# Optimization experiments

Measured on AMD Instinct MI355X. Metric: run time of the kernel, lower is better.

## Reference

```python
import jax, jax.numpy as jnp
import numpy as np
import math

B, H, S, D = 4, 16, 2048, 128

def setup_inputs() -> dict:
    key = jax.random.key(0)
    kq, kk, kv = jax.random.split(key, 3)
    query = jax.random.normal(kq, (B, H, S, D), dtype=jnp.float32)
    k = jax.random.normal(kk, (B, H, S, D), dtype=jnp.float32)
    value = jax.random.normal(kv, (B, H, S, D), dtype=jnp.float32)
    attn_mask = jnp.tril(jnp.ones((S, S), dtype=bool))  # causal
    key_padding_mask = jnp.ones((B, S), dtype=bool)      # all keys valid
    return {"query": query, "key": k, "value": value,
            "attn_mask": attn_mask, "key_padding_mask": key_padding_mask}

def reference(query, key, value, attn_mask, key_padding_mask):
    dk = query.shape[-1]
    # [B,H,Sq,Sk]
    scores = jnp.einsum('bhqd,bhkd->bhqk', query, key) / math.sqrt(dk)
    fill = jnp.finfo(scores.dtype).min
    # attn_mask [Sq,Sk] -> [1,1,Sq,Sk]; True = keep
    scores = jnp.where(attn_mask[None, None, :, :], scores, fill)
    # key_padding_mask [B,Sk] -> [B,1,1,Sk]; True = keep
    scores = jnp.where(key_padding_mask[:, None, None, :], scores, fill)
    attn = jax.nn.softmax(scores, axis=-1)
    # dropout p=0.0 / eval mode -> identity
    return jnp.einsum('bhqk,bhkd->bhqd', attn, value)
```

## Files before the change

kernel.cpp:

```cpp
#include <hip/hip_runtime.h>
#include <hip/hip_bf16.h>
#include <math.h>

#define S_LEN 2048
#define D_DIM 128
#define NHEADS 64

typedef unsigned short u16;
typedef __attribute__((ext_vector_type(8))) short bf16x8;
typedef __attribute__((ext_vector_type(4))) float f32x4;
typedef __attribute__((ext_vector_type(16))) float f32x16;

__device__ __forceinline__ u16 f2b(float f) {
  union { float f; unsigned u; } v; v.f = f;
  return (u16)((v.u + 0x7fffu + ((v.u >> 16) & 1u)) >> 16);
}
__device__ __forceinline__ unsigned pkbf(float a, float b) {
  unsigned au = __float_as_uint(a) + 0x8000u;
  unsigned bu = __float_as_uint(b) + 0x8000u;
  return (au >> 16) | (bu & 0xffff0000u);
}
__device__ __forceinline__ void pl32swap(unsigned &a, unsigned &b) {
  asm("v_permlane32_swap_b32 %0, %1" : "+v"(a), "+v"(b));
}
__device__ __forceinline__ f32x16 z16() {
  f32x16 v;
  #pragma unroll
  for (int i = 0; i < 16; ++i) v[i] = 0.f;
  return v;
}

#define GLL16(g, l) __builtin_amdgcn_global_load_lds(                       \
    (const __attribute__((address_space(1))) unsigned*)(g),                 \
    (__attribute__((address_space(3))) unsigned*)(l), 16, 0, 0)

__global__ __launch_bounds__(256, 2)
void conv_kernel(const float* __restrict__ K, const float* __restrict__ V,
                 u16* __restrict__ Kws, u16* __restrict__ Vws) {
  __shared__ __align__(16) u16 VL[128 * 72];
  const int h = blockIdx.x >> 3;
  const int s = blockIdx.x & 7;
  const int tid = threadIdx.x;
  const size_t hb = (size_t)h * S_LEN * D_DIM;
  const float* Kb = K + hb;
  const float* Vb = V + hb;
  u16* Ko = Kws + hb;
  u16* Vo = Vws + hb;

  #pragma unroll 2
  for (int it = 0; it < 16; ++it) {
    int idx = it * 256 + tid;
    int k = 256 * s + (idx >> 4), g = idx & 15;
    const float* src = Kb + (size_t)k * D_DIM + 8 * g;
    float4 a = *(const float4*)src;
    float4 b = *(const float4*)(src + 4);
    bf16x8 f;
    f[0]=f2b(a.x); f[1]=f2b(a.y); f[2]=f2b(a.z); f[3]=f2b(a.w);
    f[4]=f2b(b.x); f[5]=f2b(b.y); f[6]=f2b(b.z); f[7]=f2b(b.w);
    *(bf16x8*)&Ko[(size_t)k * D_DIM + 8 * g] = f;
  }
  for (int tt = 0; tt < 4; ++tt) {
    const int k0t = 256 * s + 64 * tt;
    __syncthreads();
    #pragma unroll 2
    for (int it = 0; it < 8; ++it) {
      int idx = it * 256 + tid;
      int row = idx >> 5, c4 = idx & 31;
      float4 v = *(const float4*)(Vb + (size_t)(k0t + row) * D_DIM + 4 * c4);
      VL[(4*c4 + 0) * 72 + row] = f2b(v.x);
      VL[(4*c4 + 1) * 72 + row] = f2b(v.y);
      VL[(4*c4 + 2) * 72 + row] = f2b(v.z);
      VL[(4*c4 + 3) * 72 + row] = f2b(v.w);
    }
    __syncthreads();
    #pragma unroll
    for (int it = 0; it < 4; ++it) {
      int idx = it * 256 + tid;
      int d = idx >> 3, kc = idx & 7;
      bf16x8 f = *(const bf16x8*)&VL[d * 72 + 8 * kc];
      *(bf16x8*)&Vo[(size_t)d * S_LEN + k0t + 8 * kc] = f;
    }
  }
}

__global__ __launch_bounds__(256, 2)
void fattn32(const float* __restrict__ Qg, const u16* __restrict__ Kws,
             const u16* __restrict__ Vws, float* __restrict__ Og) {
  __shared__ __align__(16) u16 Kl[2][8192];
  __shared__ __align__(16) u16 Vl[2][8192];

  const int tid = threadIdx.x, lane = tid & 63, w = tid >> 6;
  const int l31 = lane & 31, hi = lane >> 5;
  const int kx = l31 & 7;

  const int L = blockIdx.x;
  const int xcd = L & 7, slot = L >> 3;
  const int head = xcd * 8 + (slot >> 3);
  const int pr = slot & 7;

  const size_t hb = (size_t)head * S_LEN * D_DIM;
  const float* Qb = Qg + hb;
  float*       Ob = Og + hb;
  const u16*   Kh = Kws + hb;
  const u16*   Vh = Vws + hb;

  int cur = 0;

  auto stage = [&](int buf, int t) {
    const int k0 = t * 64;
    #pragma unroll
    for (int j = 0; j < 4; ++j) {
      const int sb = (j * 4 + w) * 64;
      {
        int sk = sb + lane;
        int k = sk >> 4, gs = sk & 15, g = gs ^ (k & 7);
        GLL16(Kh + (size_t)(k0 + k) * D_DIM + 8 * g, &Kl[buf][sb * 8]);
      }
      {
        int sv = sb + lane;
        int d = sv >> 3, gks = sv & 7, gk = gks ^ (d & 7);
        GLL16(Vh + (size_t)d * S_LEN + k0 + 8 * gk, &Vl[buf][sb * 8]);
      }
    }
  };

  #pragma unroll 1
  for (int qi = 0; qi < 2; ++qi) {
    const int qt  = qi ? pr : (15 - pr);
    const int q0w = qt * 128 + 32 * w;
    const int ntk = 2 * qt + 2;
    const int myq = q0w + l31;

    bf16x8 qf[8];
    {
      const float sc = 0.12753139f;
      const float* qp = Qb + (size_t)myq * D_DIM + 8 * hi;
      #pragma unroll
      for (int c = 0; c < 8; ++c) {
        float4 a = *(const float4*)(qp + 16 * c);
        float4 b = *(const float4*)(qp + 16 * c + 4);
        bf16x8 f;
        f[0]=f2b(a.x*sc); f[1]=f2b(a.y*sc); f[2]=f2b(a.z*sc); f[3]=f2b(a.w*sc);
        f[4]=f2b(b.x*sc); f[5]=f2b(b.y*sc); f[6]=f2b(b.z*sc); f[7]=f2b(b.w*sc);
        qf[c] = f;
      }
    }

    f32x16 oa0 = z16(), oa1 = z16(), oa2 = z16(), oa3 = z16();
    float m_run = 0.f, l_run = 0.f;

    stage(cur, 0);
    __syncthreads();

    #pragma unroll 1
    for (int t = 0; t < ntk; ++t) {
      if (t + 1 < ntk) stage(cur ^ 1, t + 1);

      if (64 * t <= q0w + 31) {
        const u16* K8 = &Kl[cur][0];
        const u16* V8 = &Vl[cur][0];

        f32x16 s0 = z16(), s1 = z16();
        __builtin_amdgcn_s_setprio(1);
        #pragma unroll
        for (int c = 0; c < 8; ++c) {
          const int gs = (c * 2 + hi) ^ kx;
          bf16x8 ka = *(const bf16x8*)&K8[ l31       * 128 + gs * 8];
          bf16x8 kb = *(const bf16x8*)&K8[(32 + l31) * 128 + gs * 8];
          s0 = __builtin_amdgcn_mfma_f32_32x32x16_bf16(ka, qf[c], s0, 0,0,0);
          s1 = __builtin_amdgcn_mfma_f32_32x32x16_bf16(kb, qf[c], s1, 0,0,0);
        }
        __builtin_amdgcn_s_setprio(0);

        if (64 * t + 63 > q0w) {
          const int qm = myq - 64 * t;
          #pragma unroll
          for (int i = 0; i < 16; ++i) {
            const int kr = (i & 3) + 8 * (i >> 2) + 4 * hi;
            if (kr > qm)      s0[i] = -1e30f;
            if (32 + kr > qm) s1[i] = -1e30f;
          }
        }

        float tm[16];
        #pragma unroll
        for (int i = 0; i < 16; ++i) tm[i] = fmaxf(s0[i], s1[i]);
        #pragma unroll
        for (int st = 8; st >= 1; st >>= 1)
          #pragma unroll
          for (int i = 0; i < 8; ++i) if (i < st) tm[i] = fmaxf(tm[i], tm[i+st]);
        float mx = fmaxf(tm[0], __shfl_xor(tm[0], 32));

        if (mx > m_run + 8.0f) {
          float corr = exp2f(m_run - mx);
          #pragma unroll
          for (int i = 0; i < 16; ++i) {
            oa0[i] *= corr; oa1[i] *= corr; oa2[i] *= corr; oa3[i] *= corr;
          }
          l_run *= corr; m_run = mx;
        }

        float ps0 = 0.f, ps1 = 0.f, ps2 = 0.f, ps3 = 0.f;
        #pragma unroll
        for (int i = 0; i < 16; ++i) {
          float p0 = exp2f(s0[i] - m_run);
          float p1 = exp2f(s1[i] - m_run);
          s0[i] = p0; s1[i] = p1;
          if ((i & 3) == 0) { ps0 += p0; ps1 += p1; }
          else if ((i & 3) == 1) { ps2 += p0; ps3 += p1; }
          else if ((i & 3) == 2) { ps0 += p0; ps1 += p1; }
          else { ps2 += p0; ps3 += p1; }
        }
        l_run += (ps0 + ps1) + (ps2 + ps3);

        unsigned w0[8], w1[8];
        #pragma unroll
        for (int j = 0; j < 8; ++j) {
          w0[j] = pkbf(s0[2*j], s0[2*j+1]);
          w1[j] = pkbf(s1[2*j], s1[2*j+1]);
        }
        pl32swap(w0[0], w0[2]); pl32swap(w0[1], w0[3]);
        pl32swap(w0[4], w0[6]); pl32swap(w0[5], w0[7]);
        pl32swap(w1[0], w1[2]); pl32swap(w1[1], w1[3]);
        pl32swap(w1[4], w1[6]); pl32swap(w1[5], w1[7]);
        union { unsigned u[4]; bf16x8 v; } pf[4];
        pf[0].u[0]=w0[0]; pf[0].u[1]=w0[1]; pf[0].u[2]=w0[2]; pf[0].u[3]=w0[3];
        pf[1].u[0]=w0[4]; pf[1].u[1]=w0[5]; pf[1].u[2]=w0[6]; pf[1].u[3]=w0[7];
        pf[2].u[0]=w1[0]; pf[2].u[1]=w1[1]; pf[2].u[2]=w1[2]; pf[2].u[3]=w1[3];
        pf[3].u[0]=w1[4]; pf[3].u[1]=w1[5]; pf[3].u[2]=w1[6]; pf[3].u[3]=w1[7];

        __builtin_amdgcn_s_setprio(1);
        #pragma unroll
        for (int c = 0; c < 4; ++c) {
          const int gv = (c * 2 + hi) ^ kx;
          bf16x8 v0 = *(const bf16x8*)&V8[( l31      ) * 64 + gv * 8];
          bf16x8 v1 = *(const bf16x8*)&V8[( 32 + l31 ) * 64 + gv * 8];
          bf16x8 v2 = *(const bf16x8*)&V8[( 64 + l31 ) * 64 + gv * 8];
          bf16x8 v3 = *(const bf16x8*)&V8[( 96 + l31 ) * 64 + gv * 8];
          oa0 = __builtin_amdgcn_mfma_f32_32x32x16_bf16(v0, pf[c].v, oa0, 0,0,0);
          oa1 = __builtin_amdgcn_mfma_f32_32x32x16_bf16(v1, pf[c].v, oa1, 0,0,0);
          oa2 = __builtin_amdgcn_mfma_f32_32x32x16_bf16(v2, pf[c].v, oa2, 0,0,0);
          oa3 = __builtin_amdgcn_mfma_f32_32x32x16_bf16(v3, pf[c].v, oa3, 0,0,0);
        }
        __builtin_amdgcn_s_setprio(0);
      }

      __syncthreads();
      cur ^= 1;
    }

    float l_tot = l_run + __shfl_xor(l_run, 32);
    float inv = 1.0f / l_tot;
    float* op = Ob + (size_t)myq * D_DIM;
    #pragma unroll
    for (int i = 0; i < 16; ++i) {
      const int d = (i & 3) + 8 * (i >> 2) + 4 * hi;
      op[d]      = oa0[i] * inv;
      op[32 + d] = oa1[i] * inv;
      op[64 + d] = oa2[i] * inv;
      op[96 + d] = oa3[i] * inv;
    }
  }
}

__global__ __launch_bounds__(256, 3)
void fattn_v2(const float* __restrict__ Qg, const float* __restrict__ Kg,
              const float* __restrict__ Vg, float* __restrict__ Og) {
  __shared__ __align__(16) u16 K8[16 * 64 * 8];
  __shared__ __align__(16) u16 V8[8 * 128 * 8];
  __shared__ __align__(16) u16 Plf[4 * 16 * 72];
  const int tid = threadIdx.x, lane = tid & 63, w = tid >> 6;
  const int lr = lane & 15, lg = lane >> 4;
  const int qtile = blockIdx.x % 32, bh = blockIdx.x / 32;
  const int q0 = qtile * 64;
  const size_t base = (size_t)bh * S_LEN * D_DIM;
  const float *Qb = Qg + base, *Kb = Kg + base, *Vb = Vg + base;
  float* Ob = Og + base;
  bf16x8 qf[4];
  {
    const float* qp = Qb + (size_t)(q0 + w * 16 + lr) * D_DIM + lg * 8;
    #pragma unroll
    for (int cc = 0; cc < 4; ++cc) {
      float4 a = *(const float4*)(qp + cc * 32);
      float4 b = *(const float4*)(qp + cc * 32 + 4);
      bf16x8 f;
      f[0]=f2b(a.x); f[1]=f2b(a.y); f[2]=f2b(a.z); f[3]=f2b(a.w);
      f[4]=f2b(b.x); f[5]=f2b(b.y); f[6]=f2b(b.z); f[7]=f2b(b.w);
      qf[cc] = f;
    }
  }
  f32x4 oacc[8];
  #pragma unroll
  for (int c = 0; c < 8; ++c) oacc[c] = (f32x4){0.f,0.f,0.f,0.f};
  float m_run[4] = {-INFINITY,-INFINITY,-INFINITY,-INFINITY};
  float l_run[4] = {0.f,0.f,0.f,0.f};
  const int sg_ = tid >> 5, dq_ = tid & 31;
  float4 kb[8], vb[8];
  auto prefetch = [&](int k0) {
    const float* kp = Kb + (size_t)(k0 + lane) * D_DIM;
    #pragma unroll
    for (int i = 0; i < 4; ++i) {
      int dg = w + 4 * i;
      kb[2*i]   = *(const float4*)(kp + dg * 8);
      kb[2*i+1] = *(const float4*)(kp + dg * 8 + 4);
    }
    #pragma unroll
    for (int jj = 0; jj < 8; ++jj) {
      int row = k0 + (jj & 3) * 16 + 2 * sg_ + (jj >> 2);
      vb[jj] = *(const float4*)(Vb + (size_t)row * D_DIM + dq_ * 4);
    }
  };
  const int ntiles = qtile + 1;
  const float scale = 0.08838834764831845f;
  prefetch(0);
  for (int t = 0; t < ntiles; ++t) {
    #pragma unroll
    for (int i = 0; i < 4; ++i) {
      int dg = w + 4 * i;
      float4 a = kb[2*i], b = kb[2*i+1];
      bf16x8 f;
      f[0]=f2b(a.x); f[1]=f2b(a.y); f[2]=f2b(a.z); f[3]=f2b(a.w);
      f[4]=f2b(b.x); f[5]=f2b(b.y); f[6]=f2b(b.z); f[7]=f2b(b.w);
      *(bf16x8*)&K8[(dg * 64 + lane) * 8] = f;
    }
    #pragma unroll
    for (int dd = 0; dd < 4; ++dd) {
      bf16x8 f;
      #pragma unroll
      for (int jj = 0; jj < 8; ++jj) {
        float c = (dd==0)?vb[jj].x:(dd==1)?vb[jj].y:(dd==2)?vb[jj].z:vb[jj].w;
        f[jj] = f2b(c);
      }
      *(bf16x8*)&V8[(sg_ * 128 + dq_ * 4 + dd) * 8] = f;
    }
    __syncthreads();
    if (t + 1 < ntiles) prefetch((t + 1) * 64);
    const bool diag = (t == qtile);
    f32x4 sa[4];
    #pragma unroll
    for (int c = 0; c < 4; ++c) sa[c] = (f32x4){0.f,0.f,0.f,0.f};
    #pragma unroll
    for (int cc = 0; cc < 4; ++cc) {
      #pragma unroll
      for (int c = 0; c < 4; ++c) {
        bf16x8 kf = *(const bf16x8*)&K8[((cc*4+lg)*64 + c*16 + lr)*8];
        sa[c] = __builtin_amdgcn_mfma_f32_16x16x32_bf16(qf[cc], kf, sa[c], 0,0,0);
      }
    }
    #pragma unroll
    for (int r = 0; r < 4; ++r) {
      float s0=sa[0][r]*scale, s1=sa[1][r]*scale, s2=sa[2][r]*scale, s3=sa[3][r]*scale;
      if (diag) {
        int lim = 16*w + lg*4 + r;
        if (     lr > lim) s0 = -INFINITY;
        if (16 + lr > lim) s1 = -INFINITY;
        if (32 + lr > lim) s2 = -INFINITY;
        if (48 + lr > lim) s3 = -INFINITY;
      }
      float mx = fmaxf(fmaxf(s0,s1), fmaxf(s2,s3));
      #pragma unroll
      for (int d = 1; d < 16; d <<= 1) mx = fmaxf(mx, __shfl_xor(mx, d));
      float mn = fmaxf(m_run[r], mx);
      float corr = __expf(m_run[r] - mn);
      float p0=__expf(s0-mn), p1=__expf(s1-mn), p2=__expf(s2-mn), p3=__expf(s3-mn);
      float ps = (p0+p1)+(p2+p3);
      #pragma unroll
      for (int d = 1; d < 16; d <<= 1) ps += __shfl_xor(ps, d);
      l_run[r] = l_run[r]*corr + ps;
      m_run[r] = mn;
      #pragma unroll
      for (int c = 0; c < 8; ++c) oacc[c][r] *= corr;
      ushort4 pw = make_ushort4(f2b(p0), f2b(p1), f2b(p2), f2b(p3));
      *(ushort4*)&Plf[((w*16 + lg*4 + r) * 72) + 4*lr] = pw;
    }
    #pragma unroll
    for (int pass = 0; pass < 2; ++pass) {
      bf16x8 pfv = *(const bf16x8*)&Plf[(w*16 + lr)*72 + pass*32 + lg*8];
      #pragma unroll
      for (int c = 0; c < 8; ++c) {
        bf16x8 vf = *(const bf16x8*)&V8[((pass*4 + lg)*128 + c*16 + lr)*8];
        oacc[c] = __builtin_amdgcn_mfma_f32_16x16x32_bf16(pfv, vf, oacc[c], 0,0,0);
      }
    }
    __syncthreads();
  }
  #pragma unroll
  for (int r = 0; r < 4; ++r) {
    const int mq = q0 + w*16 + lg*4 + r;
    const float inv = 1.0f / l_run[r];
    float* op = Ob + (size_t)mq * D_DIM + lr;
    #pragma unroll
    for (int c = 0; c < 8; ++c) op[c*16] = oacc[c][r] * inv;
  }
}

extern "C" void kernel_launch(void* const* d_in, const int* in_sizes, int n_in,
                              void* d_out, int out_size, void* d_ws, size_t ws_size,
                              hipStream_t stream) {
  const float* Q = (const float*)d_in[0];
  const float* K = (const float*)d_in[1];
  const float* V = (const float*)d_in[2];
  float* O = (float*)d_out;
  const size_t elems = (size_t)NHEADS * S_LEN * D_DIM;
  const size_t need = 2 * elems * sizeof(u16);
  if (ws_size >= need) {
    u16* Kws = (u16*)d_ws;
    u16* Vws = Kws + elems;
    conv_kernel<<<dim3(512), dim3(256), 0, stream>>>(K, V, Kws, Vws);
    fattn32<<<dim3(512), dim3(256), 0, stream>>>(Q, Kws, Vws, O);
  } else {
    fattn_v2<<<dim3(NHEADS * 32), dim3(256), 0, stream>>>(Q, K, V, O);
  }
}
```

Measured before the change: 163.9 us.

## Use 8-wave blocks with triple-buffered K/V staging and one barrier per tile

Workgroups grow from 4 to 8 waves, so each block covers a 256-row query tile and K/V tiles loaded into LDS serve twice as many queries. The double-buffered LDS ring becomes a triple buffer. Loads are issued two tiles ahead, and explicit vmcnt waits plus a single barrier per iteration replace the two __syncthreads. Together these aim to cut global/LDS traffic per query and hide load latency. The cost is 96KB of LDS per block, half as many blocks, and a coarser split of causal work across blocks.

```diff
diff --git a/kernel.cpp b/kernel.cpp
--- a/kernel.cpp
+++ b/kernel.cpp
@@ -83,11 +83,11 @@
   }
 }
 
-__global__ __launch_bounds__(256, 2)
-void fattn32(const float* __restrict__ Qg, const u16* __restrict__ Kws,
+__global__ __launch_bounds__(512, 2)
+void fattn8w(const float* __restrict__ Qg, const u16* __restrict__ Kws,
              const u16* __restrict__ Vws, float* __restrict__ Og) {
-  __shared__ __align__(16) u16 Kl[2][8192];
-  __shared__ __align__(16) u16 Vl[2][8192];
+  __shared__ __align__(16) u16 Kl[3][8192];
+  __shared__ __align__(16) u16 Vl[3][8192];
 
   const int tid = threadIdx.x, lane = tid & 63, w = tid >> 6;
   const int l31 = lane & 31, hi = lane >> 5;
@@ -95,8 +95,8 @@
 
   const int L = blockIdx.x;
   const int xcd = L & 7, slot = L >> 3;
-  const int head = xcd * 8 + (slot >> 3);
-  const int pr = slot & 7;
+  const int head = xcd * 8 + (slot >> 2);
+  const int pr = slot & 3;
 
   const size_t hb = (size_t)head * S_LEN * D_DIM;
   const float* Qb = Qg + hb;
@@ -104,13 +104,11 @@
   const u16*   Kh = Kws + hb;
   const u16*   Vh = Vws + hb;
 
-  int cur = 0;
-
   auto stage = [&](int buf, int t) {
     const int k0 = t * 64;
     #pragma unroll
-    for (int j = 0; j < 4; ++j) {
-      const int sb = (j * 4 + w) * 64;
+    for (int j = 0; j < 2; ++j) {
+      const int sb = (w * 2 + j) * 64;
       {
         int sk = sb + lane;
         int k = sk >> 4, gs = sk & 15, g = gs ^ (k & 7);
@@ -126,9 +124,9 @@
 
   #pragma unroll 1
   for (int qi = 0; qi < 2; ++qi) {
-    const int qt  = qi ? pr : (15 - pr);
-    const int q0w = qt * 128 + 32 * w;
-    const int ntk = 2 * qt + 2;
+    const int qt  = qi ? pr : (7 - pr);
+    const int q0w = qt * 256 + 32 * w;
+    const int ntk = 4 * qt + 4;
     const int myq = q0w + l31;
 
     bf16x8 qf[8];
@@ -149,16 +147,20 @@
     f32x16 oa0 = z16(), oa1 = z16(), oa2 = z16(), oa3 = z16();
     float m_run = 0.f, l_run = 0.f;
 
-    stage(cur, 0);
-    __syncthreads();
+    stage(0, 0);
+    stage(1, 1);
+    int rb = 0;
 
     #pragma unroll 1
     for (int t = 0; t < ntk; ++t) {
-      if (t + 1 < ntk) stage(cur ^ 1, t + 1);
+      if (t + 1 < ntk) asm volatile("s_waitcnt vmcnt(4)" ::: "memory");
+      else             asm volatile("s_waitcnt vmcnt(0)" ::: "memory");
+      __builtin_amdgcn_s_barrier();
+      asm volatile("" ::: "memory");
 
       if (64 * t <= q0w + 31) {
-        const u16* K8 = &Kl[cur][0];
-        const u16* V8 = &Vl[cur][0];
+        const u16* K8 = &Kl[rb][0];
+        const u16* V8 = &Vl[rb][0];
 
         f32x16 s0 = z16(), s1 = z16();
         __builtin_amdgcn_s_setprio(1);
@@ -245,8 +247,12 @@
         __builtin_amdgcn_s_setprio(0);
       }
 
-      __syncthreads();
-      cur ^= 1;
+      if (t + 2 < ntk) {
+        int nb = rb + 2; if (nb >= 3) nb -= 3;
+        stage(nb, t + 2);
+      }
+      asm volatile("" ::: "memory");
+      rb = (rb + 1 == 3) ? 0 : rb + 1;
     }
 
     float l_tot = l_run + __shfl_xor(l_run, 32);
@@ -260,6 +266,7 @@
       op[64 + d] = oa2[i] * inv;
       op[96 + d] = oa3[i] * inv;
     }
+    __builtin_amdgcn_s_barrier();
   }
 }
 
@@ -407,7 +414,7 @@
     u16* Kws = (u16*)d_ws;
     u16* Vws = Kws + elems;
     conv_kernel<<<dim3(512), dim3(256), 0, stream>>>(K, V, Kws, Vws);
-    fattn32<<<dim3(512), dim3(256), 0, stream>>>(Q, Kws, Vws, O);
+    fattn8w<<<dim3(256), dim3(512), 0, stream>>>(Q, Kws, Vws, O);
   } else {
     fattn_v2<<<dim3(NHEADS * 32), dim3(256), 0, stream>>>(Q, K, V, O);
   }
```

Measured after the change: 156.0 us. 4.8% less time.

## Split each key tile across two wave groups with LDS softmax merge

Applied to the files above, without the earlier changes.

Blocks grow from 256 to 512 threads. Each 32-row query strip is now handled by two waves that each process one 32-key half of every 64-key tile, and their partial output accumulators and running max/sum statistics are merged through LDS at the end. The bit-trick bf16 packing is replaced by the hardware v_cvt_pk_bf16_f32 instruction, and the per-tile sync becomes an explicit vmcnt wait plus barrier. The aim is more waves in flight per CU and shorter dependency chains per wave. The cost is extra LDS traffic and barriers for the final merge, plus higher register and occupancy pressure from the 512-thread launch bounds.

```diff
diff --git a/kernel.cpp b/kernel.cpp
--- a/kernel.cpp
+++ b/kernel.cpp
@@ -15,10 +15,10 @@
   union { float f; unsigned u; } v; v.f = f;
   return (u16)((v.u + 0x7fffu + ((v.u >> 16) & 1u)) >> 16);
 }
-__device__ __forceinline__ unsigned pkbf(float a, float b) {
-  unsigned au = __float_as_uint(a) + 0x8000u;
-  unsigned bu = __float_as_uint(b) + 0x8000u;
-  return (au >> 16) | (bu & 0xffff0000u);
+__device__ __forceinline__ unsigned cvtpk(float lo, float hi) {
+  unsigned r;
+  asm("v_cvt_pk_bf16_f32 %0, %1, %2" : "=v"(r) : "v"(lo), "v"(hi));
+  return r;
 }
 __device__ __forceinline__ void pl32swap(unsigned &a, unsigned &b) {
   asm("v_permlane32_swap_b32 %0, %1" : "+v"(a), "+v"(b));
@@ -83,15 +83,18 @@
   }
 }
 
-__global__ __launch_bounds__(256, 2)
-void fattn32(const float* __restrict__ Qg, const u16* __restrict__ Kws,
-             const u16* __restrict__ Vws, float* __restrict__ Og) {
-  __shared__ __align__(16) u16 Kl[2][8192];
-  __shared__ __align__(16) u16 Vl[2][8192];
+__global__ __launch_bounds__(512, 4)
+void fattn_ps(const float* __restrict__ Qg, const u16* __restrict__ Kws,
+              const u16* __restrict__ Vws, float* __restrict__ Og) {
+  __shared__ __align__(16) u16 Kl[2][2][4096];
+  __shared__ __align__(16) u16 Vl[2][2][4096];
+  __shared__ float ML[4][64];
 
   const int tid = threadIdx.x, lane = tid & 63, w = tid >> 6;
   const int l31 = lane & 31, hi = lane >> 5;
   const int kx = l31 & 7;
+  const int vx = (l31 >> 1) & 3;
+  const int strip = w & 3, par = w >> 2;
 
   const int L = blockIdx.x;
   const int xcd = L & 7, slot = L >> 3;
@@ -104,30 +107,21 @@
   const u16*   Kh = Kws + hb;
   const u16*   Vh = Vws + hb;
 
-  int cur = 0;
-
   auto stage = [&](int buf, int t) {
     const int k0 = t * 64;
     #pragma unroll
-    for (int j = 0; j < 4; ++j) {
-      const int sb = (j * 4 + w) * 64;
-      {
-        int sk = sb + lane;
-        int k = sk >> 4, gs = sk & 15, g = gs ^ (k & 7);
-        GLL16(Kh + (size_t)(k0 + k) * D_DIM + 8 * g, &Kl[buf][sb * 8]);
-      }
-      {
-        int sv = sb + lane;
-        int d = sv >> 3, gks = sv & 7, gk = gks ^ (d & 7);
-        GLL16(Vh + (size_t)d * S_LEN + k0 + 8 * gk, &Vl[buf][sb * 8]);
-      }
+    for (int j = 0; j < 2; ++j) {
+      { int k = tid >> 4, gs = tid & 15, g = gs ^ (k & 7);
+        GLL16(Kh + (size_t)(k0 + 32*j + k) * D_DIM + 8 * g, &Kl[buf][j][tid * 8]); }
+      { int d = tid >> 2, gks = tid & 3, gk = gks ^ ((d >> 1) & 3);
+        GLL16(Vh + (size_t)d * S_LEN + (k0 + 32*j) + 8 * gk, &Vl[buf][j][tid * 8]); }
     }
   };
 
   #pragma unroll 1
   for (int qi = 0; qi < 2; ++qi) {
     const int qt  = qi ? pr : (15 - pr);
-    const int q0w = qt * 128 + 32 * w;
+    const int q0w = qt * 128 + 32 * strip;
     const int ntk = 2 * qt + 2;
     const int myq = q0w + l31;
 
@@ -149,47 +143,47 @@
     f32x16 oa0 = z16(), oa1 = z16(), oa2 = z16(), oa3 = z16();
     float m_run = 0.f, l_run = 0.f;
 
-    stage(cur, 0);
-    __syncthreads();
+    stage(0, 0);
 
     #pragma unroll 1
     for (int t = 0; t < ntk; ++t) {
-      if (t + 1 < ntk) stage(cur ^ 1, t + 1);
-
-      if (64 * t <= q0w + 31) {
-        const u16* K8 = &Kl[cur][0];
-        const u16* V8 = &Vl[cur][0];
-
-        f32x16 s0 = z16(), s1 = z16();
+      asm volatile("s_waitcnt vmcnt(0)" ::: "memory");
+      __builtin_amdgcn_s_barrier();
+      asm volatile("" ::: "memory");
+      if (t + 1 < ntk) stage((t + 1) & 1, t + 1);
+
+      const int k0p = 64 * t + 32 * par;
+      if (k0p <= q0w + 31) {
+        const u16* K8 = &Kl[t & 1][par][0];
+        const u16* V8 = &Vl[t & 1][par][0];
+
+        f32x16 s = z16();
         __builtin_amdgcn_s_setprio(1);
         #pragma unroll
         for (int c = 0; c < 8; ++c) {
-          const int gs = (c * 2 + hi) ^ kx;
-          bf16x8 ka = *(const bf16x8*)&K8[ l31       * 128 + gs * 8];
-          bf16x8 kb = *(const bf16x8*)&K8[(32 + l31) * 128 + gs * 8];
-          s0 = __builtin_amdgcn_mfma_f32_32x32x16_bf16(ka, qf[c], s0, 0,0,0);
-          s1 = __builtin_amdgcn_mfma_f32_32x32x16_bf16(kb, qf[c], s1, 0,0,0);
+          const int gs = (2 * c + hi) ^ kx;
+          bf16x8 ka = *(const bf16x8*)&K8[(l31 * 16 + gs) * 8];
+          s = __builtin_amdgcn_mfma_f32_32x32x16_bf16(ka, qf[c], s, 0, 0, 0);
         }
         __builtin_amdgcn_s_setprio(0);
 
-        if (64 * t + 63 > q0w) {
-          const int qm = myq - 64 * t;
+        if (k0p + 31 > q0w) {
+          const int qm = myq - k0p;
           #pragma unroll
           for (int i = 0; i < 16; ++i) {
             const int kr = (i & 3) + 8 * (i >> 2) + 4 * hi;
-            if (kr > qm)      s0[i] = -1e30f;
-            if (32 + kr > qm) s1[i] = -1e30f;
+            if (kr > qm) s[i] = -1e30f;
           }
         }
 
-        float tm[16];
-        #pragma unroll
-        for (int i = 0; i < 16; ++i) tm[i] = fmaxf(s0[i], s1[i]);
-        #pragma unroll
-        for (int st = 8; st >= 1; st >>= 1)
-          #pragma unroll
-          for (int i = 0; i < 8; ++i) if (i < st) tm[i] = fmaxf(tm[i], tm[i+st]);
-        float mx = fmaxf(tm[0], __shfl_xor(tm[0], 32));
+        float t0 = fmaxf(s[0], s[1]),  t1 = fmaxf(s[2], s[3]);
+        float t2 = fmaxf(s[4], s[5]),  t3 = fmaxf(s[6], s[7]);
+        float t4 = fmaxf(s[8], s[9]),  t5 = fmaxf(s[10], s[11]);
+        float t6 = fmaxf(s[12], s[13]), t7 = fmaxf(s[14], s[15]);
+        t0 = fmaxf(fmaxf(t0, t1), fmaxf(t2, t3));
+        t4 = fmaxf(fmaxf(t4, t5), fmaxf(t6, t7));
+        float mx = fmaxf(t0, t4);
+        mx = fmaxf(mx, __shfl_xor(mx, 32));
 
         if (mx > m_run + 8.0f) {
           float corr = exp2f(m_run - mx);
@@ -200,66 +194,72 @@
           l_run *= corr; m_run = mx;
         }
 
-        float ps0 = 0.f, ps1 = 0.f, ps2 = 0.f, ps3 = 0.f;
-        #pragma unroll
-        for (int i = 0; i < 16; ++i) {
-          float p0 = exp2f(s0[i] - m_run);
-          float p1 = exp2f(s1[i] - m_run);
-          s0[i] = p0; s1[i] = p1;
-          if ((i & 3) == 0) { ps0 += p0; ps1 += p1; }
-          else if ((i & 3) == 1) { ps2 += p0; ps3 += p1; }
-          else if ((i & 3) == 2) { ps0 += p0; ps1 += p1; }
-          else { ps2 += p0; ps3 += p1; }
-        }
-        l_run += (ps0 + ps1) + (ps2 + ps3);
-
-        unsigned w0[8], w1[8];
+        unsigned wq[8];
+        float ps0 = 0.f, ps1 = 0.f;
         #pragma unroll
         for (int j = 0; j < 8; ++j) {
-          w0[j] = pkbf(s0[2*j], s0[2*j+1]);
-          w1[j] = pkbf(s1[2*j], s1[2*j+1]);
+          float p0 = exp2f(s[2*j]   - m_run);
+          float p1 = exp2f(s[2*j+1] - m_run);
+          ps0 += p0; ps1 += p1;
+          wq[j] = cvtpk(p0, p1);
         }
-        pl32swap(w0[0], w0[2]); pl32swap(w0[1], w0[3]);
-        pl32swap(w0[4], w0[6]); pl32swap(w0[5], w0[7]);
-        pl32swap(w1[0], w1[2]); pl32swap(w1[1], w1[3]);
-        pl32swap(w1[4], w1[6]); pl32swap(w1[5], w1[7]);
-        union { unsigned u[4]; bf16x8 v; } pf[4];
-        pf[0].u[0]=w0[0]; pf[0].u[1]=w0[1]; pf[0].u[2]=w0[2]; pf[0].u[3]=w0[3];
-        pf[1].u[0]=w0[4]; pf[1].u[1]=w0[5]; pf[1].u[2]=w0[6]; pf[1].u[3]=w0[7];
-        pf[2].u[0]=w1[0]; pf[2].u[1]=w1[1]; pf[2].u[2]=w1[2]; pf[2].u[3]=w1[3];
-        pf[3].u[0]=w1[4]; pf[3].u[1]=w1[5]; pf[3].u[2]=w1[6]; pf[3].u[3]=w1[7];
+        l_run += ps0 + ps1;
+
+        pl32swap(wq[0], wq[2]); pl32swap(wq[1], wq[3]);
+        pl32swap(wq[4], wq[6]); pl32swap(wq[5], wq[7]);
+        union { unsigned u[4]; bf16x8 v; } pf[2];
+        pf[0].u[0]=wq[0]; pf[0].u[1]=wq[1]; pf[0].u[2]=wq[2]; pf[0].u[3]=wq[3];
+        pf[1].u[0]=wq[4]; pf[1].u[1]=wq[5]; pf[1].u[2]=wq[6]; pf[1].u[3]=wq[7];
 
         __builtin_amdgcn_s_setprio(1);
         #pragma unroll
-        for (int c = 0; c < 4; ++c) {
-          const int gv = (c * 2 + hi) ^ kx;
-          bf16x8 v0 = *(const bf16x8*)&V8[( l31      ) * 64 + gv * 8];
-          bf16x8 v1 = *(const bf16x8*)&V8[( 32 + l31 ) * 64 + gv * 8];
-          bf16x8 v2 = *(const bf16x8*)&V8[( 64 + l31 ) * 64 + gv * 8];
-          bf16x8 v3 = *(const bf16x8*)&V8[( 96 + l31 ) * 64 + gv * 8];
-          oa0 = __builtin_amdgcn_mfma_f32_32x32x16_bf16(v0, pf[c].v, oa0, 0,0,0);
-          oa1 = __builtin_amdgcn_mfma_f32_32x32x16_bf16(v1, pf[c].v, oa1, 0,0,0);
-          oa2 = __builtin_amdgcn_mfma_f32_32x32x16_bf16(v2, pf[c].v, oa2, 0,0,0);
-          oa3 = __builtin_amdgcn_mfma_f32_32x32x16_bf16(v3, pf[c].v, oa3, 0,0,0);
+        for (int kc = 0; kc < 2; ++kc) {
+          const int gv = (2 * kc + hi) ^ vx;
+          bf16x8 v0 = *(const bf16x8*)&V8[(( l31      ) * 4 + gv) * 8];
+          bf16x8 v1 = *(const bf16x8*)&V8[((32 + l31) * 4 + gv) * 8];
+          bf16x8 v2 = *(const bf16x8*)&V8[((64 + l31) * 4 + gv) * 8];
+          bf16x8 v3 = *(const bf16x8*)&V8[((96 + l31) * 4 + gv) * 8];
+          oa0 = __builtin_amdgcn_mfma_f32_32x32x16_bf16(v0, pf[kc].v, oa0, 0,0,0);
+          oa1 = __builtin_amdgcn_mfma_f32_32x32x16_bf16(v1, pf[kc].v, oa1, 0,0,0);
+          oa2 = __builtin_amdgcn_mfma_f32_32x32x16_bf16(v2, pf[kc].v, oa2, 0,0,0);
+          oa3 = __builtin_amdgcn_mfma_f32_32x32x16_bf16(v3, pf[kc].v, oa3, 0,0,0);
         }
         __builtin_amdgcn_s_setprio(0);
       }
-
-      __syncthreads();
-      cur ^= 1;
-    }
-
-    float l_tot = l_run + __shfl_xor(l_run, 32);
-    float inv = 1.0f / l_tot;
-    float* op = Ob + (size_t)myq * D_DIM;
-    #pragma unroll
-    for (int i = 0; i < 16; ++i) {
-      const int d = (i & 3) + 8 * (i >> 2) + 4 * hi;
-      op[d]      = oa0[i] * inv;
-      op[32 + d] = oa1[i] * inv;
-      op[64 + d] = oa2[i] * inv;
-      op[96 + d] = oa3[i] * inv;
-    }
+    }
+
+    float l_full = l_run + __shfl_xor(l_run, 32);
+    float* MFs = (strip < 2) ? ((float*)&Kl[0][0][0] + strip * 4096)
+                             : ((float*)&Vl[0][0][0] + (strip - 2) * 4096);
+    __syncthreads();
+    if (par == 1) {
+      #pragma unroll
+      for (int i = 0; i < 16; ++i) {
+        const int R = (i & 3) + 8 * (i >> 2) + 4 * hi;
+        MFs[( 0 + R) * 32 + l31] = oa0[i];
+        MFs[(32 + R) * 32 + l31] = oa1[i];
+        MFs[(64 + R) * 32 + l31] = oa2[i];
+        MFs[(96 + R) * 32 + l31] = oa3[i];
+      }
+      if (hi == 0) { ML[strip][2 * l31] = m_run; ML[strip][2 * l31 + 1] = l_full; }
+    }
+    __syncthreads();
+    if (par == 0) {
+      const float mb = ML[strip][2 * l31], lb = ML[strip][2 * l31 + 1];
+      const float M  = fmaxf(m_run, mb);
+      const float ca = exp2f(m_run - M), cb = exp2f(mb - M);
+      const float inv = 1.0f / (l_full * ca + lb * cb);
+      float* op = Ob + (size_t)myq * D_DIM;
+      #pragma unroll
+      for (int i = 0; i < 16; ++i) {
+        const int R = (i & 3) + 8 * (i >> 2) + 4 * hi;
+        op[ 0 + R] = (oa0[i] * ca + MFs[( 0 + R) * 32 + l31] * cb) * inv;
+        op[32 + R] = (oa1[i] * ca + MFs[(32 + R) * 32 + l31] * cb) * inv;
+        op[64 + R] = (oa2[i] * ca + MFs[(64 + R) * 32 + l31] * cb) * inv;
+        op[96 + R] = (oa3[i] * ca + MFs[(96 + R) * 32 + l31] * cb) * inv;
+      }
+    }
+    __syncthreads();
   }
 }
 
@@ -407,7 +407,7 @@
     u16* Kws = (u16*)d_ws;
     u16* Vws = Kws + elems;
     conv_kernel<<<dim3(512), dim3(256), 0, stream>>>(K, V, Kws, Vws);
-    fattn32<<<dim3(512), dim3(256), 0, stream>>>(Q, Kws, Vws, O);
+    fattn_ps<<<dim3(512), dim3(512), 0, stream>>>(Q, Kws, Vws, O);
   } else {
     fattn_v2<<<dim3(NHEADS * 32), dim3(256), 0, stream>>>(Q, K, V, O);
   }
```

Result: slower. 296.5 us (+80.9%).
